# Optimization experiments

Hardware: AMD Instinct MI355X
Metric: run time of the kernel (lower is better)

The kernel has to match this reference:

```python
import jax, jax.numpy as jnp
import numpy as np

N, E = 3000, 96000
IN_C, HID, OUT_C = 512, 256, 64
K1, K2, K3 = 2000, 1000, 500  # ceil(ratio * n) per depth; ratios = [2000/N, 0.5, 0.5]


def gcn_conv(A, x, W, b):
    # GCNConv(improved=True): A_hat = A + 2I, symmetric norm; A[i, j] = weight of edge j -> i
    n = A.shape[0]
    Ah = A + 2.0 * jnp.eye(n, dtype=A.dtype)
    deg = Ah.sum(axis=1)
    dis = jnp.where(deg > 0, jax.lax.rsqrt(deg), 0.0)
    return (dis[:, None] * Ah * dis[None, :]) @ (x @ W) + b


def augment(A):
    # GraphUNet.augment_adj: add self loops, A @ A (spspmm), remove self loops
    n = A.shape[0]
    eye = jnp.eye(n, dtype=A.dtype)
    Ah = A + eye
    return (Ah @ Ah) * (1.0 - eye)


def topk_pool(A, x, w, k):
    # TopKPooling: score = tanh((x @ w) / ||w||); keep top-k nodes, scale feats, take sub-adjacency
    score = jnp.tanh((x @ w) / jnp.linalg.norm(w))
    sv, perm = jax.lax.top_k(score, k)
    return x[perm] * sv[:, None], A[perm][:, perm], perm


def setup_inputs():
    key = jax.random.key(0)
    ks = jax.random.split(key, 16)

    def glorot(k, shape):
        lim = float(np.sqrt(6.0 / (shape[0] + shape[1])))
        return jax.random.uniform(k, shape, jnp.float32, -lim, lim)

    return {
        "x": jax.random.normal(ks[0], (N, IN_C), jnp.float32),
        "edge_index": jax.random.randint(ks[1], (2, E), 0, N, jnp.int32),
        "W0": glorot(ks[2], (IN_C, HID)), "b0": jnp.zeros((HID,), jnp.float32),
        "W1": glorot(ks[3], (HID, HID)), "b1": jnp.zeros((HID,), jnp.float32),
        "W2": glorot(ks[4], (HID, HID)), "b2": jnp.zeros((HID,), jnp.float32),
        "W3": glorot(ks[5], (HID, HID)), "b3": jnp.zeros((HID,), jnp.float32),
        "p1": jax.random.normal(ks[6], (HID,), jnp.float32),
        "p2": jax.random.normal(ks[7], (HID,), jnp.float32),
        "p3": jax.random.normal(ks[8], (HID,), jnp.float32),
        "U0": glorot(ks[9], (HID, HID)), "c0": jnp.zeros((HID,), jnp.float32),
        "U1": glorot(ks[10], (HID, HID)), "c1": jnp.zeros((HID,), jnp.float32),
        "U2": glorot(ks[11], (HID, OUT_C)), "c2": jnp.zeros((OUT_C,), jnp.float32),
    }


def reference(x, edge_index, W0, b0, W1, b1, W2, b2, W3, b3, p1, p2, p3, U0, c0, U1, c1, U2, c2):
    # eval mode: dropout_edge(p=0.2) and F.dropout(p=0.92) are identity
    relu = jax.nn.relu
    src, dst = edge_index[0], edge_index[1]
    A = jnp.zeros((N, N), x.dtype).at[dst, src].add(1.0)  # dense adjacency, coalesces duplicates

    x0 = relu(gcn_conv(A, x, W0, b0))                     # down conv 0 on original graph
    x1in, A1, perm1 = topk_pool(augment(A), x0, p1, K1)
    x1 = relu(gcn_conv(A1, x1in, W1, b1))
    x2in, A2, perm2 = topk_pool(augment(A1), x1, p2, K2)
    x2 = relu(gcn_conv(A2, x2in, W2, b2))
    x3in, A3, perm3 = topk_pool(augment(A2), x2, p3, K3)
    x3 = relu(gcn_conv(A3, x3in, W3, b3))

    h = x2 + jnp.zeros_like(x2).at[perm3].set(x3)         # unpool + sum residual
    h = relu(gcn_conv(A2, h, U0, c0))
    h = x1 + jnp.zeros_like(x1).at[perm2].set(h)
    h = relu(gcn_conv(A1, h, U1, c1))
    h = x0 + jnp.zeros_like(x0).at[perm1].set(h)
    h = gcn_conv(A, h, U2, c2)                            # final up conv, no activation
    return jax.nn.log_softmax(h, axis=1)
```

## Files before the change

kernel.cpp:

```cpp
#include <hip/hip_runtime.h>
#include <math.h>
#include <stdint.h>

#define N0   3000
#define NE   96000
#define INC  512
#define HIDF 256
#define OUTC 64
#define KP1  2000
#define KP2  1000
#define KP3  500
#define KP1P 2048
#define KP2P 1024
#define KP3P 512

typedef __bf16 bf16x8 __attribute__((ext_vector_type(8)));
typedef float f32x4 __attribute__((ext_vector_type(4)));

#define GLDS16(gp, lp)                                                   \
  __builtin_amdgcn_global_load_lds(                                      \
      (__attribute__((address_space(1))) void*)(gp),                     \
      (__attribute__((address_space(3))) void*)(lp), 16, 0, 0)

static __global__ void count_k(const int* __restrict__ ei, int* __restrict__ cd) {
  int e = blockIdx.x * blockDim.x + threadIdx.x;
  if (e < NE) atomicAdd(&cd[ei[NE + e]], 1);
}

static __global__ __launch_bounds__(1024) void scan_excl_k(const int* __restrict__ cnt,
                                                           int* __restrict__ start, int n,
                                                           float* __restrict__ dis0) {
  __shared__ int s[4096];
  int tid = threadIdx.x;
  for (int i = tid; i < 4096; i += blockDim.x) s[i] = (i < n) ? cnt[i] : 0;
  __syncthreads();
  for (int d = 1; d < 4096; d <<= 1) {
    int v[4]; int r = 0;
    for (int i = tid; i < 4096; i += blockDim.x, ++r) v[r] = (i >= d) ? s[i - d] : 0;
    __syncthreads();
    r = 0;
    for (int i = tid; i < 4096; i += blockDim.x, ++r) s[i] += v[r];
    __syncthreads();
  }
  for (int i = tid; i < n; i += blockDim.x) {
    start[i] = (i == 0) ? 0 : s[i - 1];
    dis0[i] = rsqrtf((float)cnt[i] + 2.0f);
  }
  if (tid == 0) start[n] = s[n - 1];
}

static __global__ void scatter_k(const int* __restrict__ ei, const int* __restrict__ sd,
                                 int* __restrict__ fd, int* __restrict__ bd) {
  int e = blockIdx.x * blockDim.x + threadIdx.x;
  if (e < NE) {
    int d = ei[NE + e];
    bd[sd[d] + atomicAdd(&fd[d], 1)] = ei[e];
  }
}

static __global__ __launch_bounds__(256) void augA_masked_k(
    const int* __restrict__ st, const int* __restrict__ bk,
    const int* __restrict__ perm, const int* __restrict__ pos,
    __bf16* __restrict__ A1bf, float* __restrict__ dis1) {
  __shared__ float row[KP1];
  __shared__ float sh[4];
  int tid = threadIdx.x, lane = tid & 63, wave = tid >> 6;
  int r = blockIdx.x;
  int vi = perm[r];
  for (int c = tid; c < KP1; c += 256) row[c] = 0.f;
  __syncthreads();
  int b = st[vi], e = st[vi + 1];
  for (int t = b + wave; t < e; t += 4) {
    int k = bk[t];
    int jb = st[k], je = st[k + 1];
    for (int u = jb + lane; u < je; u += 64) {
      int p = pos[bk[u]];
      if (p >= 0) atomicAdd(&row[p], 1.0f);
    }
  }
  if (wave == 0)
    for (int t = b + lane; t < e; t += 64) {
      int p = pos[bk[t]];
      if (p >= 0) atomicAdd(&row[p], 2.0f);
    }
  __syncthreads();
  if (tid == 0) row[r] = 0.f;
  __syncthreads();
  float s = 0.f;
  for (int c = tid; c < KP1P; c += 256) {
    float v = (c < KP1) ? row[c] : 0.f;
    A1bf[(size_t)r * KP1P + c] = (__bf16)v;
    s += v;
  }
#pragma unroll
  for (int o = 32; o > 0; o >>= 1) s += __shfl_down(s, o, 64);
  if (lane == 0) sh[wave] = s;
  __syncthreads();
  if (tid == 0) dis1[r] = rsqrtf(sh[0] + sh[1] + sh[2] + sh[3] + 2.0f);
}

static __global__ void spmm_sc_k(const int* __restrict__ start, const int* __restrict__ idx,
                                 const float* __restrict__ xw, const float* __restrict__ dis,
                                 float* __restrict__ out, int F) {
  int row = blockIdx.x;
  int b = start[row], e = start[row + 1];
  int f = threadIdx.x;
  __shared__ int nb[256];
  __shared__ float nd[256];
  float acc = 0.f;
  for (int t0 = b; t0 < e; t0 += blockDim.x) {
    int m = min((int)blockDim.x, e - t0);
    __syncthreads();
    if (f < m) { int s = idx[t0 + f]; nb[f] = s; nd[f] = dis[s]; }
    __syncthreads();
    for (int t = 0; t < m; ++t) acc += xw[(size_t)nb[t] * F + f] * nd[t];
  }
  out[(size_t)row * F + f] = acc;
}

static __global__ void conv_hilo_k(const float* __restrict__ in, int R, int C, int Cp,
                                   __bf16* __restrict__ oh, __bf16* __restrict__ ol) {
  int idx = blockIdx.x * blockDim.x + threadIdx.x;
  if (idx < R * Cp) {
    int r = idx / Cp, c = idx - r * Cp;
    float v = (c < C) ? in[(size_t)r * C + c] : 0.f;
    __bf16 h = (__bf16)v;
    oh[idx] = h;
    if (ol) ol[idx] = (__bf16)(v - (float)h);
  }
}

struct TDesc { const float* in; __bf16* oh; __bf16* ol; int R, C, Rp; };
struct TDescs { TDesc d[7]; };
static __global__ __launch_bounds__(256) void wtconv_k(TDescs ds) {
  TDesc d = ds.d[blockIdx.z];
  int r0 = blockIdx.x * 32, c0 = blockIdx.y * 32;
  if (r0 >= d.Rp || c0 >= d.C) return;
  __shared__ float t[32][33];
  int lr = threadIdx.x >> 5, lc = threadIdx.x & 31;
#pragma unroll
  for (int i = 0; i < 4; ++i) {
    int r = r0 + lr + i * 8, c = c0 + lc;
    t[lr + i * 8][lc] = (r < d.R && c < d.C) ? d.in[(size_t)r * d.C + c] : 0.f;
  }
  __syncthreads();
#pragma unroll
  for (int i = 0; i < 4; ++i) {
    int c = c0 + lr + i * 8, r = r0 + lc;
    if (c < d.C) {
      float v = t[lc][lr + i * 8];
      __bf16 h = (__bf16)v;
      d.oh[(size_t)c * d.Rp + r] = h;
      d.ol[(size_t)c * d.Rp + r] = (__bf16)(v - (float)h);
    }
  }
}

static __global__ __launch_bounds__(256) void btrans_k(const __bf16* __restrict__ ih,
                                                       const __bf16* __restrict__ il,
                                                       __bf16* __restrict__ oh, __bf16* __restrict__ ol,
                                                       int Rin, int Ls, int Cout, int Lo) {
  __shared__ __bf16 th[32][40], tl[32][40];
  int r0 = blockIdx.x * 32, c0 = blockIdx.y * 32;
  int lr = threadIdx.x >> 5, lc = threadIdx.x & 31;
#pragma unroll
  for (int i = 0; i < 4; ++i) {
    int r = r0 + lr + i * 8, c = c0 + lc;
    bool ok = (r < Rin);
    th[lr + i * 8][lc] = ok ? ih[(size_t)r * Ls + c] : (__bf16)0.f;
    if (il) tl[lr + i * 8][lc] = ok ? il[(size_t)r * Ls + c] : (__bf16)0.f;
  }
  __syncthreads();
#pragma unroll
  for (int i = 0; i < 4; ++i) {
    int c = c0 + lr + i * 8, r = r0 + lc;
    if (c < Cout) {
      oh[(size_t)c * Lo + r] = th[lc][lr + i * 8];
      if (ol) ol[(size_t)c * Lo + r] = tl[lc][lr + i * 8];
    }
  }
}

static __global__ __launch_bounds__(256) void redtconv_k(const float* __restrict__ Cp, int ks, int mn,
                                                         int R, int C, int Rp,
                                                         __bf16* __restrict__ oh, __bf16* __restrict__ ol,
                                                         const float* __restrict__ disv,
                                                         float* __restrict__ xw_out) {
  __shared__ float t[32][33];
  int r0 = blockIdx.x * 32, c0 = blockIdx.y * 32;
  int lr = threadIdx.x >> 5, lc = threadIdx.x & 31;
#pragma unroll
  for (int i = 0; i < 4; ++i) {
    int r = r0 + lr + i * 8, c = c0 + lc;
    float v = 0.f;
    if (r < R && c < C) {
      size_t idx = (size_t)r * C + c;
      for (int z = 0; z < ks; ++z) v += Cp[(size_t)z * mn + idx];
      xw_out[idx] = v;
    }
    t[lr + i * 8][lc] = v;
  }
  __syncthreads();
#pragma unroll
  for (int i = 0; i < 4; ++i) {
    int c = c0 + lr + i * 8, r = r0 + lc;
    if (c < C) {
      float v = t[lc][lr + i * 8];
      if (r < R) v *= disv[r];
      __bf16 h = (__bf16)v;
      oh[(size_t)c * Rp + r] = h;
      ol[(size_t)c * Rp + r] = (__bf16)(v - (float)h);
    }
  }
}

static __global__ void grows2_k(const __bf16* __restrict__ s1, const __bf16* __restrict__ s2,
                                const int* __restrict__ perm, __bf16* __restrict__ d1,
                                __bf16* __restrict__ d2, int k, int L) {
  int idx = blockIdx.x * blockDim.x + threadIdx.x;
  int nv = L >> 3;
  if (idx < k * nv) {
    int r = idx / nv, c8 = (idx - r * nv) << 3;
    int sr = perm[r];
    bf16x8 v1 = *(const bf16x8*)(s1 + (size_t)sr * L + c8);
    bf16x8 v2 = *(const bf16x8*)(s2 + (size_t)sr * L + c8);
    if (sr >= c8 && sr < c8 + 8) v2[sr - c8] = (__bf16)((float)v2[sr - c8] + 2.0f);
    *(bf16x8*)(d1 + (size_t)r * L + c8) = v1;
    *(bf16x8*)(d2 + (size_t)r * L + c8) = v2;
  }
}

static __global__ void grows4_k(const __bf16* __restrict__ ah, const __bf16* __restrict__ al,
                                const __bf16* __restrict__ bh, const __bf16* __restrict__ bl,
                                const int* __restrict__ perm,
                                __bf16* __restrict__ dah, __bf16* __restrict__ dal,
                                __bf16* __restrict__ dbh, __bf16* __restrict__ dbl,
                                int k, int L) {
  int idx = blockIdx.x * blockDim.x + threadIdx.x;
  int nv = L >> 3;
  if (idx < k * nv) {
    int r = idx / nv, c8 = (idx - r * nv) << 3;
    int sr = perm[r];
    bf16x8 vah = *(const bf16x8*)(ah + (size_t)sr * L + c8);
    bf16x8 val = *(const bf16x8*)(al + (size_t)sr * L + c8);
    bf16x8 vbh = *(const bf16x8*)(bh + (size_t)sr * L + c8);
    bf16x8 vbl = *(const bf16x8*)(bl + (size_t)sr * L + c8);
    if (sr >= c8 && sr < c8 + 8) {
      int e = sr - c8;
      float v = (float)vbh[e] + (float)vbl[e] + 2.0f;
      __bf16 h = (__bf16)v;
      vbh[e] = h;
      vbl[e] = (__bf16)(v - (float)h);
    }
    *(bf16x8*)(dah + (size_t)r * L + c8) = vah;
    *(bf16x8*)(dal + (size_t)r * L + c8) = val;
    *(bf16x8*)(dbh + (size_t)r * L + c8) = vbh;
    *(bf16x8*)(dbl + (size_t)r * L + c8) = vbl;
  }
}

static __global__ void ghilo_k(const float* __restrict__ src, const int* __restrict__ perm,
                               const float* __restrict__ sv, __bf16* __restrict__ oh,
                               __bf16* __restrict__ ol, int k) {
  int idx = blockIdx.x * blockDim.x + threadIdx.x;
  if (idx < k * HIDF) {
    int r = idx >> 8;
    float v = src[(size_t)perm[r] * HIDF + (idx & 255)] * sv[r];
    __bf16 h = (__bf16)v;
    oh[idx] = h;
    ol[idx] = (__bf16)(v - (float)h);
  }
}

template <int BM, int BN>
static __global__ __launch_bounds__(256) void mgemm_k(
    const __bf16* __restrict__ A0, const __bf16* __restrict__ A1g, const __bf16* __restrict__ A2g,
    const __bf16* __restrict__ B0, const __bf16* __restrict__ B1g, const __bf16* __restrict__ B2g,
    int nseg, float* __restrict__ Cp, int M, int N, int Kp, int kchunk) {
  constexpr int FM = BM / 32, FN = BN / 32;
  __shared__ __bf16 As[2][BM * 64];
  __shared__ __bf16 Bs[2][BN * 64];
  int tid = threadIdx.x;
  int lane = tid & 63, wave = tid >> 6;
  int wx = wave & 1, wy = wave >> 1;
  int l15 = lane & 15, l4 = lane >> 4;
  int brow = blockIdx.y * BM, bcol = blockIdx.x * BN;
  int wrow = wy * (BM / 2), wcol = wx * (BN / 2);
  int srow = lane >> 3, slot = lane & 7;
  int k_beg = blockIdx.z * kchunk;
  int ksteps = kchunk >> 6;
  int nsteps = nseg * ksteps;
  const __bf16* segA[3] = {A0, A1g, A2g};
  const __bf16* segB[3] = {B0, B1g, B2g};

  auto stage = [&](int buf, int t) {
    int seg = t / ksteps;
    int k0 = k_beg + ((t - seg * ksteps) << 6);
    const __bf16* Ag = segA[seg];
    const __bf16* Bg = segB[seg];
#pragma unroll
    for (int i = 0; i < BM / 32; ++i) {
      int rl = (i * 4 + wave) * 8 + srow;
      int gr = brow + rl;
      if (gr >= M) gr = M - 1;
      int col = k0 + ((slot ^ (rl & 7)) << 3);
      GLDS16(Ag + (size_t)gr * Kp + col, &As[buf][(i * 4 + wave) * 8 * 64]);
    }
#pragma unroll
    for (int i = 0; i < BN / 32; ++i) {
      int rl = (i * 4 + wave) * 8 + srow;
      int gc = bcol + rl;
      if (gc >= N) gc = N - 1;
      int col = k0 + ((slot ^ (rl & 7)) << 3);
      GLDS16(Bg + (size_t)gc * Kp + col, &Bs[buf][(i * 4 + wave) * 8 * 64]);
    }
  };

  f32x4 acc[FM][FN] = {};
  stage(0, 0);
  __syncthreads();
  int cur = 0;
  for (int t = 0; t < nsteps; ++t) {
    if (t + 1 < nsteps) stage(cur ^ 1, t + 1);
#pragma unroll
    for (int sub = 0; sub < 2; ++sub) {
      bf16x8 af[FM], bfv[FN];
#pragma unroll
      for (int i = 0; i < FM; ++i) {
        int r = wrow + i * 16 + l15;
        af[i] = *(const bf16x8*)(&As[cur][r * 64 + (((sub * 4 + l4) ^ (r & 7)) << 3)]);
      }
#pragma unroll
      for (int j = 0; j < FN; ++j) {
        int r = wcol + j * 16 + l15;
        bfv[j] = *(const bf16x8*)(&Bs[cur][r * 64 + (((sub * 4 + l4) ^ (r & 7)) << 3)]);
      }
#pragma unroll
      for (int i = 0; i < FM; ++i)
#pragma unroll
        for (int j = 0; j < FN; ++j)
          acc[i][j] = __builtin_amdgcn_mfma_f32_16x16x32_bf16(af[i], bfv[j], acc[i][j], 0, 0, 0);
    }
    __syncthreads();
    cur ^= 1;
  }
  size_t zoff = (size_t)blockIdx.z * M * N;
#pragma unroll
  for (int i = 0; i < FM; ++i)
#pragma unroll
    for (int j = 0; j < FN; ++j) {
      int col = bcol + wcol + j * 16 + l15;
      if (col < N) {
#pragma unroll
        for (int q = 0; q < 4; ++q) {
          int row = brow + wrow + i * 16 + l4 * 4 + q;
          if (row < M) Cp[zoff + (size_t)row * N + col] = acc[i][j][q];
        }
      }
    }
}

static __global__ void reduce_k(const float* __restrict__ p, int ks, int mn, float* __restrict__ out) {
  int idx = blockIdx.x * blockDim.x + threadIdx.x;
  if (idx < mn) {
    float s = 0.f;
    for (int z = 0; z < ks; ++z) s += p[(size_t)z * mn + idx];
    out[idx] = s;
  }
}

static __global__ void conv_epi_k(const float* __restrict__ zp, int ks, int mn,
                                  const float* __restrict__ xw, const float* __restrict__ dis,
                                  const float* __restrict__ b, float* __restrict__ out,
                                  int n, int f, int relu) {
  int idx = blockIdx.x * blockDim.x + threadIdx.x;
  if (idx < n * f) {
    float zv = 0.f;
    for (int z = 0; z < ks; ++z) zv += zp[(size_t)z * mn + idx];
    int i = idx / f, j = idx - i * f;
    float di = dis[i];
    float v = di * zv + 2.0f * di * di * xw[idx] + b[j];
    if (relu) v = fmaxf(v, 0.0f);
    out[idx] = v;
  }
}

static __global__ __launch_bounds__(256) void aug_epi_k(const float* __restrict__ Cp, int ks, int mn,
                                                        int n, int Kpad,
                                                        __bf16* __restrict__ bh, __bf16* __restrict__ bl,
                                                        float* __restrict__ dis) {
  __shared__ float sh[4];
  int r = blockIdx.x;
  int tid = threadIdx.x, lane = tid & 63, wave = tid >> 6;
  float ssum = 0.f;
  for (int c = tid; c < Kpad; c += 256) {
    float v = 0.f;
    if (c < n && c != r)
      for (int z = 0; z < ks; ++z) v += Cp[(size_t)z * mn + (size_t)r * n + c];
    __bf16 h = (__bf16)v;
    bh[(size_t)r * Kpad + c] = h;
    bl[(size_t)r * Kpad + c] = (__bf16)(v - (float)h);
    ssum += v;
  }
#pragma unroll
  for (int o = 32; o > 0; o >>= 1) ssum += __shfl_down(ssum, o, 64);
  if (lane == 0) sh[wave] = ssum;
  __syncthreads();
  if (tid == 0) dis[r] = rsqrtf(sh[0] + sh[1] + sh[2] + sh[3] + 2.0f);
}

static __global__ void score_k(const float* __restrict__ x, const float* __restrict__ w,
                               float* __restrict__ sc, int f) {
  int row = blockIdx.x;
  float s = 0.f, q = 0.f;
  for (int j = threadIdx.x; j < f; j += blockDim.x) {
    float wv = w[j];
    q += wv * wv;
    s += x[(size_t)row * f + j] * wv;
  }
  __shared__ float sh[8], sh2[8];
  int lane = threadIdx.x & 63, wid = threadIdx.x >> 6;
#pragma unroll
  for (int o = 32; o > 0; o >>= 1) { s += __shfl_down(s, o, 64); q += __shfl_down(q, o, 64); }
  if (lane == 0) { sh[wid] = s; sh2[wid] = q; }
  __syncthreads();
  if (threadIdx.x == 0) {
    float t = 0.f, t2 = 0.f;
    int nw = (blockDim.x + 63) >> 6;
    for (int w2 = 0; w2 < nw; ++w2) { t += sh[w2]; t2 += sh2[w2]; }
    sc[row] = tanhf(t / sqrtf(t2));
  }
}

static __global__ __launch_bounds__(256) void topk_rank_k(const float* __restrict__ sc, int n, int k,
                                                          int* __restrict__ perm, float* __restrict__ sv,
                                                          int* __restrict__ pos) {
  __shared__ float s[N0 + 8];
  int tid = threadIdx.x, lane = tid & 63, wave = tid >> 6;
  for (int i = tid; i < n; i += 256) s[i] = sc[i];
  __syncthreads();
  int i = blockIdx.x * 4 + wave;
  if (i < n) {
    float si = s[i];
    int rank = 0;
    for (int j = lane; j < n; j += 64) {
      float sj = s[j];
      rank += (sj > si) || (sj == si && j < i);
    }
#pragma unroll
    for (int o = 32; o > 0; o >>= 1) rank += __shfl_down(rank, o, 64);
    if (lane == 0) {
      pos[i] = (rank < k) ? rank : -1;
      if (rank < k) { perm[rank] = i; sv[rank] = si; }
    }
  }
}

static __global__ void unpool_hilo_k(const float* __restrict__ base, const float* __restrict__ up,
                                     const int* __restrict__ pos, __bf16* __restrict__ oh,
                                     __bf16* __restrict__ ol, int n) {
  int idx = blockIdx.x * blockDim.x + threadIdx.x;
  if (idx < n * HIDF) {
    int i = idx >> 8;
    int p = pos[i];
    float v = base[idx] + (p >= 0 ? up[(size_t)p * HIDF + (idx & 255)] : 0.f);
    __bf16 h = (__bf16)v;
    oh[idx] = h;
    ol[idx] = (__bf16)(v - (float)h);
  }
}

static __global__ void epilsm_k(const float* __restrict__ zb, const float* __restrict__ xw,
                                const float* __restrict__ dis, const float* __restrict__ b,
                                float* __restrict__ out) {
  int r = blockIdx.x, j = threadIdx.x;
  float di = dis[r];
  float v = di * zb[r * OUTC + j] + 2.0f * di * di * xw[r * OUTC + j] + b[j];
  float m = v;
#pragma unroll
  for (int o = 32; o > 0; o >>= 1) m = fmaxf(m, __shfl_xor(m, o, 64));
  float e = expf(v - m), s = e;
#pragma unroll
  for (int o = 32; o > 0; o >>= 1) s += __shfl_xor(s, o, 64);
  out[r * OUTC + j] = v - m - logf(s);
}

extern "C" void kernel_launch(void* const* d_in, const int* in_sizes, int n_in,
                              void* d_out, int out_size, void* d_ws, size_t ws_size,
                              hipStream_t stream) {
  const float* x  = (const float*)d_in[0];
  const int* ei   = (const int*)d_in[1];
  const float* W0 = (const float*)d_in[2];
  const float* b0 = (const float*)d_in[3];
  const float* W1 = (const float*)d_in[4];
  const float* b1 = (const float*)d_in[5];
  const float* W2 = (const float*)d_in[6];
  const float* b2 = (const float*)d_in[7];
  const float* W3 = (const float*)d_in[8];
  const float* b3 = (const float*)d_in[9];
  const float* p1 = (const float*)d_in[10];
  const float* p2 = (const float*)d_in[11];
  const float* p3 = (const float*)d_in[12];
  const float* U0 = (const float*)d_in[13];
  const float* c0 = (const float*)d_in[14];
  const float* U1 = (const float*)d_in[15];
  const float* c1 = (const float*)d_in[16];
  const float* U2 = (const float*)d_in[17];
  const float* c2 = (const float*)d_in[18];
  (void)in_sizes; (void)n_in; (void)out_size; (void)ws_size;

  char* basep = (char*)d_ws;
  size_t off = 0;
  auto alloc = [&](size_t bytes) {
    void* p = basep + off;
    off += (bytes + 255) & ~(size_t)255;
    return p;
  };

  float* xw  = (float*)alloc((size_t)N0 * HIDF * 4);
  float* zb  = (float*)alloc((size_t)N0 * HIDF * 4);
  float* x0  = (float*)alloc((size_t)N0 * HIDF * 4);
  float* x1  = (float*)alloc((size_t)KP1 * HIDF * 4);
  float* x2  = (float*)alloc((size_t)KP2 * HIDF * 4);
  float* x3  = (float*)alloc((size_t)KP3 * HIDF * 4);
  float* hb  = (float*)alloc((size_t)N0 * HIDF * 4);
  float* Cpart = (float*)alloc((size_t)20 * 1024 * 1024);
  __bf16* bfAh = (__bf16*)alloc((size_t)N0 * INC * 2);
  __bf16* bfAl = (__bf16*)alloc((size_t)N0 * INC * 2);
  __bf16* bfBh = (__bf16*)alloc((size_t)HIDF * KP1P * 2);
  __bf16* bfBl = (__bf16*)alloc((size_t)HIDF * KP1P * 2);
  __bf16* A1bf  = (__bf16*)alloc((size_t)KP1 * KP1P * 2);
  __bf16* A1tbf = (__bf16*)alloc((size_t)KP1 * KP1P * 2);
  __bf16* Ag    = (__bf16*)alloc((size_t)KP2 * KP1P * 2);
  __bf16* Bg    = (__bf16*)alloc((size_t)KP2 * KP1P * 2);
  __bf16* A2bh  = (__bf16*)alloc((size_t)KP2 * KP2P * 2);
  __bf16* A2bl  = (__bf16*)alloc((size_t)KP2 * KP2P * 2);
  __bf16* A2tbh = (__bf16*)alloc((size_t)KP2 * KP2P * 2);
  __bf16* A2tbl = (__bf16*)alloc((size_t)KP2 * KP2P * 2);
  __bf16* Agh   = (__bf16*)alloc((size_t)KP3 * KP2P * 2);
  __bf16* Agl   = (__bf16*)alloc((size_t)KP3 * KP2P * 2);
  __bf16* Bgh   = (__bf16*)alloc((size_t)KP3 * KP2P * 2);
  __bf16* Bgl   = (__bf16*)alloc((size_t)KP3 * KP2P * 2);
  __bf16* A3bh  = (__bf16*)alloc((size_t)KP3 * KP3P * 2);
  __bf16* A3bl  = (__bf16*)alloc((size_t)KP3 * KP3P * 2);
  __bf16* w0h = (__bf16*)alloc((size_t)HIDF * 512 * 2);
  __bf16* w0l = (__bf16*)alloc((size_t)HIDF * 512 * 2);
  __bf16* w1h = (__bf16*)alloc((size_t)HIDF * 256 * 2);
  __bf16* w1l = (__bf16*)alloc((size_t)HIDF * 256 * 2);
  __bf16* w2h = (__bf16*)alloc((size_t)HIDF * 256 * 2);
  __bf16* w2l = (__bf16*)alloc((size_t)HIDF * 256 * 2);
  __bf16* w3h = (__bf16*)alloc((size_t)HIDF * 256 * 2);
  __bf16* w3l = (__bf16*)alloc((size_t)HIDF * 256 * 2);
  __bf16* u0h = (__bf16*)alloc((size_t)HIDF * 256 * 2);
  __bf16* u0l = (__bf16*)alloc((size_t)HIDF * 256 * 2);
  __bf16* u1h = (__bf16*)alloc((size_t)HIDF * 256 * 2);
  __bf16* u1l = (__bf16*)alloc((size_t)HIDF * 256 * 2);
  __bf16* u2h = (__bf16*)alloc((size_t)OUTC * 256 * 2);
  __bf16* u2l = (__bf16*)alloc((size_t)OUTC * 256 * 2);
  float* sc   = (float*)alloc(N0 * 4);
  float* sv   = (float*)alloc(KP1 * 4);
  int* perm1  = (int*)alloc(KP1 * 4);
  int* perm2  = (int*)alloc(KP2 * 4);
  int* perm3  = (int*)alloc(KP3 * 4);
  int* pos1   = (int*)alloc(N0 * 4);
  int* pos2   = (int*)alloc(KP1 * 4);
  int* pos3   = (int*)alloc(KP2 * 4);
  float* dis0 = (float*)alloc(N0 * 4);
  float* dis1 = (float*)alloc(KP1 * 4);
  float* dis2 = (float*)alloc(KP2 * 4);
  float* dis3 = (float*)alloc(KP3 * 4);
  int* cf     = (int*)alloc((size_t)2 * 3072 * 4);
  int* cnt_d  = cf;
  int* fl_d   = cf + 3072;
  int* st_d   = (int*)alloc((N0 + 4) * 4);
  int* bk_d   = (int*)alloc(NE * 4);

  auto mg = [&](int bm, int bn, const __bf16* a0, const __bf16* a1, const __bf16* a2,
                const __bf16* bb0, const __bf16* bb1, const __bf16* bb2,
                int nseg, int M, int N, int Kp, int ks, int kchunk) {
    dim3 g((N + bn - 1) / bn, (M + bm - 1) / bm, ks);
    if (bm == 128 && bn == 128)
      mgemm_k<128, 128><<<g, 256, 0, stream>>>(a0, a1, a2, bb0, bb1, bb2, nseg, Cpart, M, N, Kp, kchunk);
    else if (bm == 128)
      mgemm_k<128, 64><<<g, 256, 0, stream>>>(a0, a1, a2, bb0, bb1, bb2, nseg, Cpart, M, N, Kp, kchunk);
    else
      mgemm_k<64, 64><<<g, 256, 0, stream>>>(a0, a1, a2, bb0, bb1, bb2, nseg, Cpart, M, N, Kp, kchunk);
  };

  auto wgemm = [&](const __bf16* wh, const __bf16* wl, int fin, int fout, int n, int bm,
                   int ks, int kchunk) {
    int Kp = (fin + 63) & ~63;
    mg(bm, 64, bfAh, bfAh, bfAl, wh, wl, wh, 3, n, fout, Kp, ks, kchunk);
  };

  auto prop = [&](int ksw, const __bf16* Abh, const __bf16* Abl, int asegs, int n, int Kp, int bm,
                  int ks, int kchunk, const float* disv, const float* bias, float* outx, int relu) {
    dim3 tg(Kp / 32, HIDF / 32);
    redtconv_k<<<tg, 256, 0, stream>>>(Cpart, ksw, n * HIDF, n, HIDF, Kp, bfBh, bfBl, disv, xw);
    if (asegs == 1) mg(bm, 64, Abh, Abh, nullptr, bfBh, bfBl, nullptr, 2, n, HIDF, Kp, ks, kchunk);
    else            mg(bm, 64, Abh, Abh, Abl, bfBh, bfBl, bfBh, 3, n, HIDF, Kp, ks, kchunk);
    conv_epi_k<<<(n * HIDF + 255) / 256, 256, 0, stream>>>(Cpart, ks, n * HIDF, xw, disv, bias,
                                                           outx, n, HIDF, relu);
  };

  auto pool = [&](const float* xfeat, int n, const float* p, int k, int* perm, int* pos) {
    score_k<<<n, 256, 0, stream>>>(xfeat, p, sc, HIDF);
    topk_rank_k<<<(n + 3) / 4, 256, 0, stream>>>(sc, n, k, perm, sv, pos);
  };

  hipMemsetAsync(cf, 0, (size_t)2 * 3072 * 4, stream);
  count_k<<<(NE + 255) / 256, 256, 0, stream>>>(ei, cnt_d);
  {
    TDescs ds;
    ds.d[0] = {W0, w0h, w0l, INC, HIDF, 512};
    ds.d[1] = {W1, w1h, w1l, HIDF, HIDF, 256};
    ds.d[2] = {W2, w2h, w2l, HIDF, HIDF, 256};
    ds.d[3] = {W3, w3h, w3l, HIDF, HIDF, 256};
    ds.d[4] = {U0, u0h, u0l, HIDF, HIDF, 256};
    ds.d[5] = {U1, u1h, u1l, HIDF, HIDF, 256};
    ds.d[6] = {U2, u2h, u2l, HIDF, OUTC, 256};
    wtconv_k<<<dim3(16, 8, 7), 256, 0, stream>>>(ds);
  }
  scan_excl_k<<<1, 1024, 0, stream>>>(cnt_d, st_d, N0, dis0);
  scatter_k<<<(NE + 255) / 256, 256, 0, stream>>>(ei, st_d, fl_d, bk_d);

  conv_hilo_k<<<((size_t)N0 * INC + 255) / 256, 256, 0, stream>>>(x, N0, INC, INC, bfAh, bfAl);
  wgemm(w0h, w0l, INC, HIDF, N0, 128, 4, 128);
  reduce_k<<<(N0 * HIDF + 255) / 256, 256, 0, stream>>>(Cpart, 4, N0 * HIDF, xw);
  spmm_sc_k<<<N0, HIDF, 0, stream>>>(st_d, bk_d, xw, dis0, zb, HIDF);
  conv_epi_k<<<(N0 * HIDF + 255) / 256, 256, 0, stream>>>(zb, 1, 0, xw, dis0, b0, x0, N0, HIDF, 1);

  pool(x0, N0, p1, KP1, perm1, pos1);
  augA_masked_k<<<KP1, 256, 0, stream>>>(st_d, bk_d, perm1, pos1, A1bf, dis1);

  ghilo_k<<<((size_t)KP1 * HIDF + 255) / 256, 256, 0, stream>>>(x0, perm1, sv, bfAh, bfAl, KP1);
  wgemm(w1h, w1l, HIDF, HIDF, KP1, 128, 4, 64);
  prop(4, A1bf, nullptr, 1, KP1, KP1P, 128, 4, 512, dis1, b1, x1, 1);

  pool(x1, KP1, p2, KP2, perm2, pos2);
  btrans_k<<<dim3(KP1P / 32, (KP1 + 31) / 32), 256, 0, stream>>>(A1bf, nullptr, A1tbf, nullptr,
                                                                 KP1, KP1P, KP1, KP1P);
  grows2_k<<<((size_t)KP2 * (KP1P / 8) + 255) / 256, 256, 0, stream>>>(A1bf, A1tbf, perm2, Ag, Bg,
                                                                       KP2, KP1P);
  mg(128, 128, Ag, nullptr, nullptr, Bg, nullptr, nullptr, 1, KP2, KP2, KP1P, 4, 512);
  aug_epi_k<<<KP2, 256, 0, stream>>>(Cpart, 4, KP2 * KP2, KP2, KP2P, A2bh, A2bl, dis2);

  ghilo_k<<<((size_t)KP2 * HIDF + 255) / 256, 256, 0, stream>>>(x1, perm2, sv, bfAh, bfAl, KP2);
  wgemm(w2h, w2l, HIDF, HIDF, KP2, 64, 4, 64);
  prop(4, A2bh, A2bl, 2, KP2, KP2P, 128, 8, 128, dis2, b2, x2, 1);

  pool(x2, KP2, p3, KP3, perm3, pos3);
  btrans_k<<<dim3(KP2P / 32, (KP2 + 31) / 32), 256, 0, stream>>>(A2bh, A2bl, A2tbh, A2tbl,
                                                                 KP2, KP2P, KP2, KP2P);
  grows4_k<<<((size_t)KP3 * (KP2P / 8) + 255) / 256, 256, 0, stream>>>(
      A2bh, A2bl, A2tbh, A2tbl, perm3, Agh, Agl, Bgh, Bgl, KP3, KP2P);
  mg(64, 64, Agh, Agh, Agl, Bgh, Bgl, Bgh, 3, KP3, KP3, KP2P, 4, 256);
  aug_epi_k<<<KP3, 256, 0, stream>>>(Cpart, 4, KP3 * KP3, KP3, KP3P, A3bh, A3bl, dis3);

  ghilo_k<<<((size_t)KP3 * HIDF + 255) / 256, 256, 0, stream>>>(x2, perm3, sv, bfAh, bfAl, KP3);
  wgemm(w3h, w3l, HIDF, HIDF, KP3, 64, 4, 64);
  prop(4, A3bh, A3bl, 2, KP3, KP3P, 64, 8, 64, dis3, b3, x3, 1);

  unpool_hilo_k<<<(KP2 * HIDF + 255) / 256, 256, 0, stream>>>(x2, x3, pos3, bfAh, bfAl, KP2);
  wgemm(u0h, u0l, HIDF, HIDF, KP2, 64, 4, 64);
  prop(4, A2bh, A2bl, 2, KP2, KP2P, 128, 8, 128, dis2, c0, hb, 1);

  unpool_hilo_k<<<(KP1 * HIDF + 255) / 256, 256, 0, stream>>>(x1, hb, pos2, bfAh, bfAl, KP1);
  wgemm(u1h, u1l, HIDF, HIDF, KP1, 128, 4, 64);
  prop(4, A1bf, nullptr, 1, KP1, KP1P, 128, 4, 512, dis1, c1, hb, 1);

  unpool_hilo_k<<<(N0 * HIDF + 255) / 256, 256, 0, stream>>>(x0, hb, pos1, bfAh, bfAl, N0);
  wgemm(u2h, u2l, HIDF, OUTC, N0, 64, 4, 64);
  reduce_k<<<(N0 * OUTC + 255) / 256, 256, 0, stream>>>(Cpart, 4, N0 * OUTC, xw);
  spmm_sc_k<<<N0, OUTC, 0, stream>>>(st_d, bk_d, xw, dis0, zb, OUTC);
  epilsm_k<<<N0, OUTC, 0, stream>>>(zb, xw, dis0, c2, (float*)d_out);
}
```

Before: 450.1 us.

## Fuse conv epilogues with scoring/unpool and gather pooled rows inside GEMM

Folds the conv epilogue into the top-k score computation and into the unpool+hi/lo split kernels, removing the separate conv_epi, score and unpool passes and their intermediate buffers. It also drops the grows2/grows4 row-gather kernels: mgemm now indexes rows through permutation arrays while loading tiles. The +2I correction moves into aug_epi, which reads the source row into shared memory. The goal is fewer kernel launches and less global traffic, at the cost of indirect loads inside the GEMM staging and larger epilogue kernels.

```diff
diff --git a/kernel.cpp b/kernel.cpp
--- a/kernel.cpp
+++ b/kernel.cpp
@@ -214,51 +214,6 @@
   }
 }
 
-static __global__ void grows2_k(const __bf16* __restrict__ s1, const __bf16* __restrict__ s2,
-                                const int* __restrict__ perm, __bf16* __restrict__ d1,
-                                __bf16* __restrict__ d2, int k, int L) {
-  int idx = blockIdx.x * blockDim.x + threadIdx.x;
-  int nv = L >> 3;
-  if (idx < k * nv) {
-    int r = idx / nv, c8 = (idx - r * nv) << 3;
-    int sr = perm[r];
-    bf16x8 v1 = *(const bf16x8*)(s1 + (size_t)sr * L + c8);
-    bf16x8 v2 = *(const bf16x8*)(s2 + (size_t)sr * L + c8);
-    if (sr >= c8 && sr < c8 + 8) v2[sr - c8] = (__bf16)((float)v2[sr - c8] + 2.0f);
-    *(bf16x8*)(d1 + (size_t)r * L + c8) = v1;
-    *(bf16x8*)(d2 + (size_t)r * L + c8) = v2;
-  }
-}
-
-static __global__ void grows4_k(const __bf16* __restrict__ ah, const __bf16* __restrict__ al,
-                                const __bf16* __restrict__ bh, const __bf16* __restrict__ bl,
-                                const int* __restrict__ perm,
-                                __bf16* __restrict__ dah, __bf16* __restrict__ dal,
-                                __bf16* __restrict__ dbh, __bf16* __restrict__ dbl,
-                                int k, int L) {
-  int idx = blockIdx.x * blockDim.x + threadIdx.x;
-  int nv = L >> 3;
-  if (idx < k * nv) {
-    int r = idx / nv, c8 = (idx - r * nv) << 3;
-    int sr = perm[r];
-    bf16x8 vah = *(const bf16x8*)(ah + (size_t)sr * L + c8);
-    bf16x8 val = *(const bf16x8*)(al + (size_t)sr * L + c8);
-    bf16x8 vbh = *(const bf16x8*)(bh + (size_t)sr * L + c8);
-    bf16x8 vbl = *(const bf16x8*)(bl + (size_t)sr * L + c8);
-    if (sr >= c8 && sr < c8 + 8) {
-      int e = sr - c8;
-      float v = (float)vbh[e] + (float)vbl[e] + 2.0f;
-      __bf16 h = (__bf16)v;
-      vbh[e] = h;
-      vbl[e] = (__bf16)(v - (float)h);
-    }
-    *(bf16x8*)(dah + (size_t)r * L + c8) = vah;
-    *(bf16x8*)(dal + (size_t)r * L + c8) = val;
-    *(bf16x8*)(dbh + (size_t)r * L + c8) = vbh;
-    *(bf16x8*)(dbl + (size_t)r * L + c8) = vbl;
-  }
-}
-
 static __global__ void ghilo_k(const float* __restrict__ src, const int* __restrict__ perm,
                                const float* __restrict__ sv, __bf16* __restrict__ oh,
                                __bf16* __restrict__ ol, int k) {
@@ -276,6 +231,7 @@
 static __global__ __launch_bounds__(256) void mgemm_k(
     const __bf16* __restrict__ A0, const __bf16* __restrict__ A1g, const __bf16* __restrict__ A2g,
     const __bf16* __restrict__ B0, const __bf16* __restrict__ B1g, const __bf16* __restrict__ B2g,
+    const int* __restrict__ pA, const int* __restrict__ pB,
     int nseg, float* __restrict__ Cp, int M, int N, int Kp, int kchunk) {
   constexpr int FM = BM / 32, FN = BN / 32;
   __shared__ __bf16 As[2][BM * 64];
@@ -303,6 +259,7 @@
       int rl = (i * 4 + wave) * 8 + srow;
       int gr = brow + rl;
       if (gr >= M) gr = M - 1;
+      if (pA) gr = pA[gr];
       int col = k0 + ((slot ^ (rl & 7)) << 3);
       GLDS16(Ag + (size_t)gr * Kp + col, &As[buf][(i * 4 + wave) * 8 * 64]);
     }
@@ -311,6 +268,7 @@
       int rl = (i * 4 + wave) * 8 + srow;
       int gc = bcol + rl;
       if (gc >= N) gc = N - 1;
+      if (pB) gc = pB[gc];
       int col = k0 + ((slot ^ (rl & 7)) << 3);
       GLDS16(Bg + (size_t)gc * Kp + col, &Bs[buf][(i * 4 + wave) * 8 * 64]);
     }
@@ -369,37 +327,82 @@
   }
 }
 
-static __global__ void conv_epi_k(const float* __restrict__ zp, int ks, int mn,
-                                  const float* __restrict__ xw, const float* __restrict__ dis,
-                                  const float* __restrict__ b, float* __restrict__ out,
-                                  int n, int f, int relu) {
+static __global__ __launch_bounds__(256) void epi_score_k(
+    const float* __restrict__ zp, int ks, int mn, const float* __restrict__ xw,
+    const float* __restrict__ disv, const float* __restrict__ bias,
+    const float* __restrict__ p, float* __restrict__ outx, float* __restrict__ sc) {
+  int r = blockIdx.x, tid = threadIdx.x;
+  size_t idx = (size_t)r * HIDF + tid;
+  float zv = 0.f;
+  for (int z = 0; z < ks; ++z) zv += zp[(size_t)z * mn + idx];
+  float di = disv[r];
+  float v = di * zv + 2.0f * di * di * xw[idx] + bias[tid];
+  v = fmaxf(v, 0.0f);
+  outx[idx] = v;
+  float wv = p[tid];
+  float s = v * wv, q = wv * wv;
+  __shared__ float sh[4], sh2[4];
+  int lane = tid & 63, wid = tid >> 6;
+#pragma unroll
+  for (int o = 32; o > 0; o >>= 1) { s += __shfl_down(s, o, 64); q += __shfl_down(q, o, 64); }
+  if (lane == 0) { sh[wid] = s; sh2[wid] = q; }
+  __syncthreads();
+  if (tid == 0)
+    sc[r] = tanhf((sh[0] + sh[1] + sh[2] + sh[3]) / sqrtf(sh2[0] + sh2[1] + sh2[2] + sh2[3]));
+}
+
+static __global__ void unpool_epi_k(const float* __restrict__ base, const float* __restrict__ zp,
+                                    int ks, int mn, const float* __restrict__ xwp,
+                                    const float* __restrict__ disv, const float* __restrict__ bias,
+                                    const int* __restrict__ pos, __bf16* __restrict__ oh,
+                                    __bf16* __restrict__ ol, int n) {
   int idx = blockIdx.x * blockDim.x + threadIdx.x;
-  if (idx < n * f) {
-    float zv = 0.f;
-    for (int z = 0; z < ks; ++z) zv += zp[(size_t)z * mn + idx];
-    int i = idx / f, j = idx - i * f;
-    float di = dis[i];
-    float v = di * zv + 2.0f * di * di * xw[idx] + b[j];
-    if (relu) v = fmaxf(v, 0.0f);
-    out[idx] = v;
-  }
-}
-
-static __global__ __launch_bounds__(256) void aug_epi_k(const float* __restrict__ Cp, int ks, int mn,
-                                                        int n, int Kpad,
-                                                        __bf16* __restrict__ bh, __bf16* __restrict__ bl,
-                                                        float* __restrict__ dis) {
+  if (idx < n * HIDF) {
+    int i = idx >> 8, j = idx & 255;
+    int p = pos[i];
+    float v = base[idx];
+    if (p >= 0) {
+      size_t pidx = (size_t)p * HIDF + j;
+      float zv = 0.f;
+      for (int z = 0; z < ks; ++z) zv += zp[(size_t)z * mn + pidx];
+      float di = disv[p];
+      float u = di * zv + 2.0f * di * di * xwp[pidx] + bias[j];
+      v += fmaxf(u, 0.0f);
+    }
+    __bf16 h = (__bf16)v;
+    oh[idx] = h;
+    ol[idx] = (__bf16)(v - (float)h);
+  }
+}
+
+static __global__ __launch_bounds__(256) void aug_epi_k(
+    const float* __restrict__ Cp, int ks, int mn, int n, int dstL,
+    const __bf16* __restrict__ srcH, const __bf16* __restrict__ srcL, int srcLen,
+    const int* __restrict__ permv, __bf16* __restrict__ bh, __bf16* __restrict__ bl,
+    float* __restrict__ dis) {
+  __shared__ int pm[1000];
+  __shared__ float srow[2048];
   __shared__ float sh[4];
   int r = blockIdx.x;
   int tid = threadIdx.x, lane = tid & 63, wave = tid >> 6;
+  int vi = permv[r];
+  for (int c = tid; c < n; c += 256) pm[c] = permv[c];
+  for (int k = tid; k < srcLen; k += 256) {
+    float v = (float)srcH[(size_t)vi * srcLen + k];
+    if (srcL) v += (float)srcL[(size_t)vi * srcLen + k];
+    srow[k] = v;
+  }
+  __syncthreads();
   float ssum = 0.f;
-  for (int c = tid; c < Kpad; c += 256) {
+  for (int c = tid; c < dstL; c += 256) {
     float v = 0.f;
-    if (c < n && c != r)
+    if (c < n && c != r) {
       for (int z = 0; z < ks; ++z) v += Cp[(size_t)z * mn + (size_t)r * n + c];
+      v += 2.0f * srow[pm[c]];
+    }
     __bf16 h = (__bf16)v;
-    bh[(size_t)r * Kpad + c] = h;
-    bl[(size_t)r * Kpad + c] = (__bf16)(v - (float)h);
+    bh[(size_t)r * dstL + c] = h;
+    bl[(size_t)r * dstL + c] = (__bf16)(v - (float)h);
     ssum += v;
   }
 #pragma unroll
@@ -407,29 +410,6 @@
   if (lane == 0) sh[wave] = ssum;
   __syncthreads();
   if (tid == 0) dis[r] = rsqrtf(sh[0] + sh[1] + sh[2] + sh[3] + 2.0f);
-}
-
-static __global__ void score_k(const float* __restrict__ x, const float* __restrict__ w,
-                               float* __restrict__ sc, int f) {
-  int row = blockIdx.x;
-  float s = 0.f, q = 0.f;
-  for (int j = threadIdx.x; j < f; j += blockDim.x) {
-    float wv = w[j];
-    q += wv * wv;
-    s += x[(size_t)row * f + j] * wv;
-  }
-  __shared__ float sh[8], sh2[8];
-  int lane = threadIdx.x & 63, wid = threadIdx.x >> 6;
-#pragma unroll
-  for (int o = 32; o > 0; o >>= 1) { s += __shfl_down(s, o, 64); q += __shfl_down(q, o, 64); }
-  if (lane == 0) { sh[wid] = s; sh2[wid] = q; }
-  __syncthreads();
-  if (threadIdx.x == 0) {
-    float t = 0.f, t2 = 0.f;
-    int nw = (blockDim.x + 63) >> 6;
-    for (int w2 = 0; w2 < nw; ++w2) { t += sh[w2]; t2 += sh2[w2]; }
-    sc[row] = tanhf(t / sqrtf(t2));
-  }
 }
 
 static __global__ __launch_bounds__(256) void topk_rank_k(const float* __restrict__ sc, int n, int k,
@@ -453,20 +433,6 @@
       pos[i] = (rank < k) ? rank : -1;
       if (rank < k) { perm[rank] = i; sv[rank] = si; }
     }
-  }
-}
-
-static __global__ void unpool_hilo_k(const float* __restrict__ base, const float* __restrict__ up,
-                                     const int* __restrict__ pos, __bf16* __restrict__ oh,
-                                     __bf16* __restrict__ ol, int n) {
-  int idx = blockIdx.x * blockDim.x + threadIdx.x;
-  if (idx < n * HIDF) {
-    int i = idx >> 8;
-    int p = pos[i];
-    float v = base[idx] + (p >= 0 ? up[(size_t)p * HIDF + (idx & 255)] : 0.f);
-    __bf16 h = (__bf16)v;
-    oh[idx] = h;
-    ol[idx] = (__bf16)(v - (float)h);
   }
 }
 
@@ -522,8 +488,6 @@
   float* x0  = (float*)alloc((size_t)N0 * HIDF * 4);
   float* x1  = (float*)alloc((size_t)KP1 * HIDF * 4);
   float* x2  = (float*)alloc((size_t)KP2 * HIDF * 4);
-  float* x3  = (float*)alloc((size_t)KP3 * HIDF * 4);
-  float* hb  = (float*)alloc((size_t)N0 * HIDF * 4);
   float* Cpart = (float*)alloc((size_t)20 * 1024 * 1024);
   __bf16* bfAh = (__bf16*)alloc((size_t)N0 * INC * 2);
   __bf16* bfAl = (__bf16*)alloc((size_t)N0 * INC * 2);
@@ -531,16 +495,10 @@
   __bf16* bfBl = (__bf16*)alloc((size_t)HIDF * KP1P * 2);
   __bf16* A1bf  = (__bf16*)alloc((size_t)KP1 * KP1P * 2);
   __bf16* A1tbf = (__bf16*)alloc((size_t)KP1 * KP1P * 2);
-  __bf16* Ag    = (__bf16*)alloc((size_t)KP2 * KP1P * 2);
-  __bf16* Bg    = (__bf16*)alloc((size_t)KP2 * KP1P * 2);
   __bf16* A2bh  = (__bf16*)alloc((size_t)KP2 * KP2P * 2);
   __bf16* A2bl  = (__bf16*)alloc((size_t)KP2 * KP2P * 2);
   __bf16* A2tbh = (__bf16*)alloc((size_t)KP2 * KP2P * 2);
   __bf16* A2tbl = (__bf16*)alloc((size_t)KP2 * KP2P * 2);
-  __bf16* Agh   = (__bf16*)alloc((size_t)KP3 * KP2P * 2);
-  __bf16* Agl   = (__bf16*)alloc((size_t)KP3 * KP2P * 2);
-  __bf16* Bgh   = (__bf16*)alloc((size_t)KP3 * KP2P * 2);
-  __bf16* Bgl   = (__bf16*)alloc((size_t)KP3 * KP2P * 2);
   __bf16* A3bh  = (__bf16*)alloc((size_t)KP3 * KP3P * 2);
   __bf16* A3bl  = (__bf16*)alloc((size_t)KP3 * KP3P * 2);
   __bf16* w0h = (__bf16*)alloc((size_t)HIDF * 512 * 2);
@@ -577,35 +535,29 @@
 
   auto mg = [&](int bm, int bn, const __bf16* a0, const __bf16* a1, const __bf16* a2,
                 const __bf16* bb0, const __bf16* bb1, const __bf16* bb2,
+                const int* pA, const int* pB,
                 int nseg, int M, int N, int Kp, int ks, int kchunk) {
     dim3 g((N + bn - 1) / bn, (M + bm - 1) / bm, ks);
     if (bm == 128 && bn == 128)
-      mgemm_k<128, 128><<<g, 256, 0, stream>>>(a0, a1, a2, bb0, bb1, bb2, nseg, Cpart, M, N, Kp, kchunk);
+      mgemm_k<128, 128><<<g, 256, 0, stream>>>(a0, a1, a2, bb0, bb1, bb2, pA, pB, nseg, Cpart, M, N, Kp, kchunk);
     else if (bm == 128)
-      mgemm_k<128, 64><<<g, 256, 0, stream>>>(a0, a1, a2, bb0, bb1, bb2, nseg, Cpart, M, N, Kp, kchunk);
+      mgemm_k<128, 64><<<g, 256, 0, stream>>>(a0, a1, a2, bb0, bb1, bb2, pA, pB, nseg, Cpart, M, N, Kp, kchunk);
     else
-      mgemm_k<64, 64><<<g, 256, 0, stream>>>(a0, a1, a2, bb0, bb1, bb2, nseg, Cpart, M, N, Kp, kchunk);
+      mgemm_k<64, 64><<<g, 256, 0, stream>>>(a0, a1, a2, bb0, bb1, bb2, pA, pB, nseg, Cpart, M, N, Kp, kchunk);
   };
 
   auto wgemm = [&](const __bf16* wh, const __bf16* wl, int fin, int fout, int n, int bm,
                    int ks, int kchunk) {
     int Kp = (fin + 63) & ~63;
-    mg(bm, 64, bfAh, bfAh, bfAl, wh, wl, wh, 3, n, fout, Kp, ks, kchunk);
+    mg(bm, 64, bfAh, bfAh, bfAl, wh, wl, wh, nullptr, nullptr, 3, n, fout, Kp, ks, kchunk);
   };
 
-  auto prop = [&](int ksw, const __bf16* Abh, const __bf16* Abl, int asegs, int n, int Kp, int bm,
-                  int ks, int kchunk, const float* disv, const float* bias, float* outx, int relu) {
+  auto propg = [&](int ksw, const __bf16* Abh, const __bf16* Abl, int asegs, int n, int Kp, int bm,
+                   int ks, int kchunk, const float* disv) {
     dim3 tg(Kp / 32, HIDF / 32);
     redtconv_k<<<tg, 256, 0, stream>>>(Cpart, ksw, n * HIDF, n, HIDF, Kp, bfBh, bfBl, disv, xw);
-    if (asegs == 1) mg(bm, 64, Abh, Abh, nullptr, bfBh, bfBl, nullptr, 2, n, HIDF, Kp, ks, kchunk);
-    else            mg(bm, 64, Abh, Abh, Abl, bfBh, bfBl, bfBh, 3, n, HIDF, Kp, ks, kchunk);
-    conv_epi_k<<<(n * HIDF + 255) / 256, 256, 0, stream>>>(Cpart, ks, n * HIDF, xw, disv, bias,
-                                                           outx, n, HIDF, relu);
-  };
-
-  auto pool = [&](const float* xfeat, int n, const float* p, int k, int* perm, int* pos) {
-    score_k<<<n, 256, 0, stream>>>(xfeat, p, sc, HIDF);
-    topk_rank_k<<<(n + 3) / 4, 256, 0, stream>>>(sc, n, k, perm, sv, pos);
+    if (asegs == 1) mg(bm, 64, Abh, Abh, nullptr, bfBh, bfBl, nullptr, nullptr, nullptr, 2, n, HIDF, Kp, ks, kchunk);
+    else            mg(bm, 64, Abh, Abh, Abl, bfBh, bfBl, bfBh, nullptr, nullptr, 3, n, HIDF, Kp, ks, kchunk);
   };
 
   hipMemsetAsync(cf, 0, (size_t)2 * 3072 * 4, stream);
@@ -628,48 +580,52 @@
   wgemm(w0h, w0l, INC, HIDF, N0, 128, 4, 128);
   reduce_k<<<(N0 * HIDF + 255) / 256, 256, 0, stream>>>(Cpart, 4, N0 * HIDF, xw);
   spmm_sc_k<<<N0, HIDF, 0, stream>>>(st_d, bk_d, xw, dis0, zb, HIDF);
-  conv_epi_k<<<(N0 * HIDF + 255) / 256, 256, 0, stream>>>(zb, 1, 0, xw, dis0, b0, x0, N0, HIDF, 1);
-
-  pool(x0, N0, p1, KP1, perm1, pos1);
+  epi_score_k<<<N0, 256, 0, stream>>>(zb, 1, 0, xw, dis0, b0, p1, x0, sc);
+  topk_rank_k<<<(N0 + 3) / 4, 256, 0, stream>>>(sc, N0, KP1, perm1, sv, pos1);
+
   augA_masked_k<<<KP1, 256, 0, stream>>>(st_d, bk_d, perm1, pos1, A1bf, dis1);
 
   ghilo_k<<<((size_t)KP1 * HIDF + 255) / 256, 256, 0, stream>>>(x0, perm1, sv, bfAh, bfAl, KP1);
   wgemm(w1h, w1l, HIDF, HIDF, KP1, 128, 4, 64);
-  prop(4, A1bf, nullptr, 1, KP1, KP1P, 128, 4, 512, dis1, b1, x1, 1);
-
-  pool(x1, KP1, p2, KP2, perm2, pos2);
+  propg(4, A1bf, nullptr, 1, KP1, KP1P, 128, 4, 512, dis1);
+  epi_score_k<<<KP1, 256, 0, stream>>>(Cpart, 4, KP1 * HIDF, xw, dis1, b1, p2, x1, sc);
+  topk_rank_k<<<(KP1 + 3) / 4, 256, 0, stream>>>(sc, KP1, KP2, perm2, sv, pos2);
+
   btrans_k<<<dim3(KP1P / 32, (KP1 + 31) / 32), 256, 0, stream>>>(A1bf, nullptr, A1tbf, nullptr,
                                                                  KP1, KP1P, KP1, KP1P);
-  grows2_k<<<((size_t)KP2 * (KP1P / 8) + 255) / 256, 256, 0, stream>>>(A1bf, A1tbf, perm2, Ag, Bg,
-                                                                       KP2, KP1P);
-  mg(128, 128, Ag, nullptr, nullptr, Bg, nullptr, nullptr, 1, KP2, KP2, KP1P, 4, 512);
-  aug_epi_k<<<KP2, 256, 0, stream>>>(Cpart, 4, KP2 * KP2, KP2, KP2P, A2bh, A2bl, dis2);
+  mg(128, 128, A1bf, nullptr, nullptr, A1tbf, nullptr, nullptr, perm2, perm2,
+     1, KP2, KP2, KP1P, 4, 512);
+  aug_epi_k<<<KP2, 256, 0, stream>>>(Cpart, 4, KP2 * KP2, KP2, KP2P, A1bf, nullptr, KP1P, perm2,
+                                     A2bh, A2bl, dis2);
 
   ghilo_k<<<((size_t)KP2 * HIDF + 255) / 256, 256, 0, stream>>>(x1, perm2, sv, bfAh, bfAl, KP2);
   wgemm(w2h, w2l, HIDF, HIDF, KP2, 64, 4, 64);
-  prop(4, A2bh, A2bl, 2, KP2, KP2P, 128, 8, 128, dis2, b2, x2, 1);
-
-  pool(x2, KP2, p3, KP3, perm3, pos3);
+  propg(4, A2bh, A2bl, 2, KP2, KP2P, 128, 8, 128, dis2);
+  epi_score_k<<<KP2, 256, 0, stream>>>(Cpart, 8, KP2 * HIDF, xw, dis2, b2, p3, x2, sc);
+  topk_rank_k<<<(KP2 + 3) / 4, 256, 0, stream>>>(sc, KP2, KP3, perm3, sv, pos3);
+
   btrans_k<<<dim3(KP2P / 32, (KP2 + 31) / 32), 256, 0, stream>>>(A2bh, A2bl, A2tbh, A2tbl,
                                                                  KP2, KP2P, KP2, KP2P);
-  grows4_k<<<((size_t)KP3 * (KP2P / 8) + 255) / 256, 256, 0, stream>>>(
-      A2bh, A2bl, A2tbh, A2tbl, perm3, Agh, Agl, Bgh, Bgl, KP3, KP2P);
-  mg(64, 64, Agh, Agh, Agl, Bgh, Bgl, Bgh, 3, KP3, KP3, KP2P, 4, 256);
-  aug_epi_k<<<KP3, 256, 0, stream>>>(Cpart, 4, KP3 * KP3, KP3, KP3P, A3bh, A3bl, dis3);
+  mg(64, 64, A2bh, A2bh, A2bl, A2tbh, A2tbl, A2tbh, perm3, perm3, 3, KP3, KP3, KP2P, 4, 256);
+  aug_epi_k<<<KP3, 256, 0, stream>>>(Cpart, 4, KP3 * KP3, KP3, KP3P, A2bh, A2bl, KP2P, perm3,
+                                     A3bh, A3bl, dis3);
 
   ghilo_k<<<((size_t)KP3 * HIDF + 255) / 256, 256, 0, stream>>>(x2, perm3, sv, bfAh, bfAl, KP3);
   wgemm(w3h, w3l, HIDF, HIDF, KP3, 64, 4, 64);
-  prop(4, A3bh, A3bl, 2, KP3, KP3P, 64, 8, 64, dis3, b3, x3, 1);
-
-  unpool_hilo_k<<<(KP2 * HIDF + 255) / 256, 256, 0, stream>>>(x2, x3, pos3, bfAh, bfAl, KP2);
+  propg(4, A3bh, A3bl, 2, KP3, KP3P, 64, 8, 64, dis3);
+  unpool_epi_k<<<(KP2 * HIDF + 255) / 256, 256, 0, stream>>>(x2, Cpart, 8, KP3 * HIDF, xw, dis3, b3,
+                                                             pos3, bfAh, bfAl, KP2);
+
   wgemm(u0h, u0l, HIDF, HIDF, KP2, 64, 4, 64);
-  prop(4, A2bh, A2bl, 2, KP2, KP2P, 128, 8, 128, dis2, c0, hb, 1);
-
-  unpool_hilo_k<<<(KP1 * HIDF + 255) / 256, 256, 0, stream>>>(x1, hb, pos2, bfAh, bfAl, KP1);
+  propg(4, A2bh, A2bl, 2, KP2, KP2P, 128, 8, 128, dis2);
+  unpool_epi_k<<<(KP1 * HIDF + 255) / 256, 256, 0, stream>>>(x1, Cpart, 8, KP2 * HIDF, xw, dis2, c0,
+                                                             pos2, bfAh, bfAl, KP1);
+
   wgemm(u1h, u1l, HIDF, HIDF, KP1, 128, 4, 64);
-  prop(4, A1bf, nullptr, 1, KP1, KP1P, 128, 4, 512, dis1, c1, hb, 1);
-
-  unpool_hilo_k<<<(N0 * HIDF + 255) / 256, 256, 0, stream>>>(x0, hb, pos1, bfAh, bfAl, N0);
+  propg(4, A1bf, nullptr, 1, KP1, KP1P, 128, 4, 512, dis1);
+  unpool_epi_k<<<(N0 * HIDF + 255) / 256, 256, 0, stream>>>(x0, Cpart, 4, KP1 * HIDF, xw, dis1, c1,
+                                                            pos1, bfAh, bfAl, N0);
+
   wgemm(u2h, u2l, HIDF, OUTC, N0, 64, 4, 64);
   reduce_k<<<(N0 * OUTC + 255) / 256, 256, 0, stream>>>(Cpart, 4, N0 * OUTC, xw);
   spmm_sc_k<<<N0, OUTC, 0, stream>>>(st_d, bk_d, xw, dis0, zb, OUTC);
```

After: 450.5 us. About the same (+0.1%).
